# Performance work log

Hardware: AMD Instinct MI355X
Metric: run time of the kernel (lower is better)

## Reference

```python
import jax, jax.numpy as jnp
import numpy as np

NUM_HEADS = 32
NUM_KV_HEADS = 8
HEAD_DIM = 128
SEQ = 2048
MASK_BLOCK = 128  # diffusion-LM denoising block size


def setup_inputs() -> dict:
    key = jax.random.key(0)
    kq, kk, kv = jax.random.split(key, 3)
    q = jax.random.normal(kq, (SEQ, NUM_HEADS * HEAD_DIM), dtype=jnp.float32)
    k = jax.random.normal(kk, (SEQ, NUM_KV_HEADS * HEAD_DIM), dtype=jnp.float32)
    v = jax.random.normal(kv, (SEQ, NUM_KV_HEADS * HEAD_DIM), dtype=jnp.float32)
    # block-causal mask at MASK_BLOCK granularity: token_q attends to token_kv
    # iff block(token_kv) <= block(token_q). Every row has >=1 True entry.
    blk = jnp.arange(SEQ) // MASK_BLOCK
    block_mask = blk[None, :] <= blk[:, None]  # [S, S] bool
    return {"q": q, "k": k, "v": v, "block_mask": block_mask}


def reference(q, k, v, block_mask):
    S = q.shape[0]
    scale = 1.0 / np.sqrt(HEAD_DIM).astype(np.float32)  # flex_attention default scale
    qh = q.reshape(S, NUM_HEADS, HEAD_DIM)       # [S, Hq, D]
    kh = k.reshape(S, NUM_KV_HEADS, HEAD_DIM)    # [S, Hkv, D]
    vh = v.reshape(S, NUM_KV_HEADS, HEAD_DIM)
    # GQA: repeat each kv head over its query-head group
    group = NUM_HEADS // NUM_KV_HEADS
    kh = jnp.repeat(kh, group, axis=1)           # [S, Hq, D]
    vh = jnp.repeat(vh, group, axis=1)
    scores = jnp.einsum('qhd,khd->hqk', qh, kh) * scale  # [Hq, S, S]
    neg_inf = jnp.finfo(scores.dtype).min
    scores = jnp.where(block_mask[None, :, :], scores, neg_inf)
    probs = jax.nn.softmax(scores, axis=-1)
    o = jnp.einsum('hqk,khd->qhd', probs, vh)    # [S, Hq, D]
    return o.reshape(S, NUM_HEADS * HEAD_DIM)
```

## Files before the change

kernel.cpp:

```cpp
#include <hip/hip_runtime.h>
#include <hip/hip_bf16.h>

#define SEQL  2048
#define NHQ   32
#define NHKV  8
#define HD    128

typedef __attribute__((ext_vector_type(4))) float          f32x4;
typedef __attribute__((ext_vector_type(8))) short          bf16x8;
typedef __attribute__((ext_vector_type(4))) unsigned short u16x4;
typedef __attribute__((ext_vector_type(8))) unsigned short u16x8;
typedef __attribute__((ext_vector_type(2))) unsigned int   u32x2;

__device__ __forceinline__ unsigned short f2bf(float f) {
  union { float f; unsigned u; } v; v.f = f;
  unsigned u = v.u;
  return (unsigned short)((u + 0x7fffu + ((u >> 16) & 1u)) >> 16);
}

__device__ __forceinline__ void gload16(const void* g, void* l) {
  __builtin_amdgcn_global_load_lds(
      (const __attribute__((address_space(1))) unsigned int*)g,
      (__attribute__((address_space(3))) unsigned int*)l, 16, 0, 0);
}

__global__ __launch_bounds__(256) void prep_k(const float* __restrict__ k,
                                              unsigned short* __restrict__ kws) {
  int t = blockIdx.x * 256 + threadIdx.x;
  int s   = t >> 7;
  int col = (t & 127) << 3;
  int hkv = col >> 7;
  int d0  = col & 127;
  const float* src = k + (size_t)s * (NHKV * HD) + col;
  f32x4 a = *(const f32x4*)src;
  f32x4 b = *(const f32x4*)(src + 4);
  u16x8 r;
  r[0] = f2bf(a[0]); r[1] = f2bf(a[1]); r[2] = f2bf(a[2]); r[3] = f2bf(a[3]);
  r[4] = f2bf(b[0]); r[5] = f2bf(b[1]); r[6] = f2bf(b[2]); r[7] = f2bf(b[3]);
  int tile = s >> 6, rr = s & 63;
  int idx = (rr * 128 + d0) ^ ((rr & 7) << 3);
  *(u16x8*)(kws + (((size_t)(hkv * 32 + tile)) << 13) + idx) = r;
}

__global__ __launch_bounds__(256) void prep_v(const float* __restrict__ v,
                                              unsigned short* __restrict__ vws) {
  int t = blockIdx.x * 256 + threadIdx.x;
  int d   = t & 127;
  int hkv = (t >> 7) & 7;
  int rg  = t >> 10;
  int s0  = rg << 3;
  const float* src = v + (size_t)s0 * (NHKV * HD) + hkv * HD + d;
  u16x8 r;
  #pragma unroll
  for (int j = 0; j < 8; ++j) r[j] = f2bf(src[(size_t)j * (NHKV * HD)]);
  int tile = rg >> 3;
  int rloc = (rg & 7) << 3;
  int idx = (d * 64 + rloc) ^ ((d & 7) << 3);
  *(u16x8*)(vws + (((size_t)(hkv * 32 + tile)) << 13) + idx) = r;
}

__global__ __launch_bounds__(256, 2) void attn_fwd3(
    const float* __restrict__ q,
    const unsigned short* __restrict__ kws,
    const unsigned short* __restrict__ vws,
    float* __restrict__ out)
{
  __shared__ unsigned short Kb[2][8192];
  __shared__ unsigned short Vb[2][8192];
  __shared__ unsigned int   Pst[4][1024];

  const int tid  = threadIdx.x;
  const int lane = tid & 63;
  const int wv   = tid >> 6;
  const int l15  = lane & 15;
  const int lhi  = lane >> 4;
  const int swzP = (l15 & 7) << 2;
  const int swzK = (l15 & 7) << 3;

  const int bx   = blockIdx.x;
  const int hkv  = bx & 7;
  const int idx2 = bx >> 3;
  const int h    = hkv * 4 + (idx2 & 3);
  const int qt   = 15 - (idx2 >> 2);
  const int nt   = 2 * (qt + 1);

  const float qscale = 0.08838834764831845f * 1.4426950408889634f;
  const float THR = 11.5f;

  const unsigned short* ktiles = kws + (((size_t)hkv * 32) << 13);
  const unsigned short* vtiles = vws + (((size_t)hkv * 32) << 13);

  bf16x8 qf[2][4];
  #pragma unroll
  for (int qs = 0; qs < 2; ++qs) {
    const float* qbase = q + (size_t)(qt * 128 + qs * 64 + wv * 16 + l15) * (NHQ * HD) + h * HD + lhi * 8;
    #pragma unroll
    for (int c = 0; c < 4; ++c) {
      f32x4 a = *(const f32x4*)(qbase + c * 32);
      f32x4 b = *(const f32x4*)(qbase + c * 32 + 4);
      bf16x8 r;
      r[0] = (short)f2bf(a[0] * qscale);
      r[1] = (short)f2bf(a[1] * qscale);
      r[2] = (short)f2bf(a[2] * qscale);
      r[3] = (short)f2bf(a[3] * qscale);
      r[4] = (short)f2bf(b[0] * qscale);
      r[5] = (short)f2bf(b[1] * qscale);
      r[6] = (short)f2bf(b[2] * qscale);
      r[7] = (short)f2bf(b[3] * qscale);
      qf[qs][c] = r;
    }
  }

  f32x4 oacc[2][8];
  #pragma unroll
  for (int qs = 0; qs < 2; ++qs)
    #pragma unroll
    for (int i = 0; i < 8; ++i) oacc[qs][i] = (f32x4){0.f, 0.f, 0.f, 0.f};
  float mrun0 = -1e30f, mrun1 = -1e30f, lrun0 = 0.f, lrun1 = 0.f;

  auto STAGE = [&](int b, int kvt) {
    const char* gk = (const char*)(ktiles + ((size_t)kvt << 13));
    const char* gv = (const char*)(vtiles + ((size_t)kvt << 13));
    char* lk = (char*)&Kb[b][0];
    char* lv = (char*)&Vb[b][0];
    #pragma unroll
    for (int i = 0; i < 4; ++i) {
      const int off = wv * 4096 + i * 1024;
      gload16(gk + off + lane * 16, lk + off);
      gload16(gv + off + lane * 16, lv + off);
    }
  };

  auto compute = [&](int b) {
    f32x4 sa0[4], sa1[4];
    #pragma unroll
    for (int sub = 0; sub < 4; ++sub) {
      f32x4 a0 = (f32x4){0.f, 0.f, 0.f, 0.f};
      f32x4 a1 = (f32x4){0.f, 0.f, 0.f, 0.f};
      const int row = sub * 16 + l15;
      #pragma unroll
      for (int c = 0; c < 4; ++c) {
        bf16x8 kf = *(const bf16x8*)(&Kb[b][(row * 128 + c * 32 + lhi * 8) ^ swzK]);
        a0 = __builtin_amdgcn_mfma_f32_16x16x32_bf16(kf, qf[0][c], a0, 0, 0, 0);
        a1 = __builtin_amdgcn_mfma_f32_16x16x32_bf16(kf, qf[1][c], a1, 0, 0, 0);
      }
      sa0[sub] = a0; sa1[sub] = a1;
    }
    float mt0 = -1e30f, mt1 = -1e30f;
    #pragma unroll
    for (int sub = 0; sub < 4; ++sub)
      #pragma unroll
      for (int r = 0; r < 4; ++r) {
        mt0 = fmaxf(mt0, sa0[sub][r]);
        mt1 = fmaxf(mt1, sa1[sub][r]);
      }
    mt0 = fmaxf(mt0, __shfl_xor(mt0, 16));
    mt0 = fmaxf(mt0, __shfl_xor(mt0, 32));
    mt1 = fmaxf(mt1, __shfl_xor(mt1, 16));
    mt1 = fmaxf(mt1, __shfl_xor(mt1, 32));
    int need = (mt0 > mrun0 + THR) || (mt1 > mrun1 + THR);
    if (__any(need)) {
      float mn0 = fmaxf(mrun0, mt0), mn1 = fmaxf(mrun1, mt1);
      float c0 = exp2f(mrun0 - mn0), c1 = exp2f(mrun1 - mn1);
      mrun0 = mn0; mrun1 = mn1;
      lrun0 *= c0; lrun1 *= c1;
      #pragma unroll
      for (int d = 0; d < 8; ++d) { oacc[0][d] *= c0; oacc[1][d] *= c1; }
    }
    {
      float ts = 0.f;
      #pragma unroll
      for (int sub = 0; sub < 4; ++sub) {
        float p0 = exp2f(sa0[sub][0] - mrun0);
        float p1 = exp2f(sa0[sub][1] - mrun0);
        float p2 = exp2f(sa0[sub][2] - mrun0);
        float p3 = exp2f(sa0[sub][3] - mrun0);
        ts += (p0 + p1) + (p2 + p3);
        u32x2 w;
        w[0] = (unsigned)f2bf(p0) | ((unsigned)f2bf(p1) << 16);
        w[1] = (unsigned)f2bf(p2) | ((unsigned)f2bf(p3) << 16);
        *(u32x2*)(&Pst[wv][(l15 * 32 + sub * 8 + lhi * 2) ^ swzP]) = w;
      }
      ts += __shfl_xor(ts, 16);
      ts += __shfl_xor(ts, 32);
      lrun0 += ts;
    }
    {
      float ts = 0.f;
      #pragma unroll
      for (int sub = 0; sub < 4; ++sub) {
        float p0 = exp2f(sa1[sub][0] - mrun1);
        float p1 = exp2f(sa1[sub][1] - mrun1);
        float p2 = exp2f(sa1[sub][2] - mrun1);
        float p3 = exp2f(sa1[sub][3] - mrun1);
        ts += (p0 + p1) + (p2 + p3);
        u32x2 w;
        w[0] = (unsigned)f2bf(p0) | ((unsigned)f2bf(p1) << 16);
        w[1] = (unsigned)f2bf(p2) | ((unsigned)f2bf(p3) << 16);
        *(u32x2*)(&Pst[wv][(512 + l15 * 32 + sub * 8 + lhi * 2) ^ swzP]) = w;
      }
      ts += __shfl_xor(ts, 16);
      ts += __shfl_xor(ts, 32);
      lrun1 += ts;
    }
    #pragma unroll
    for (int kc = 0; kc < 2; ++kc) {
      bf16x8 pf0 = *(const bf16x8*)(&Pst[wv][(l15 * 32 + kc * 16 + lhi * 4) ^ swzP]);
      bf16x8 pf1 = *(const bf16x8*)(&Pst[wv][(512 + l15 * 32 + kc * 16 + lhi * 4) ^ swzP]);
      #pragma unroll
      for (int dsub = 0; dsub < 8; ++dsub) {
        const int d = dsub * 16 + l15;
        bf16x8 vf = *(const bf16x8*)(&Vb[b][(d * 64 + kc * 32 + lhi * 8) ^ swzK]);
        oacc[0][dsub] = __builtin_amdgcn_mfma_f32_16x16x32_bf16(vf, pf0, oacc[0][dsub], 0, 0, 0);
        oacc[1][dsub] = __builtin_amdgcn_mfma_f32_16x16x32_bf16(vf, pf1, oacc[1][dsub], 0, 0, 0);
      }
    }
  };

  STAGE(0, 0);
  int buf = 0;
  for (int t = 0; t < nt; ++t) {
    if (t + 1 < nt) {
      STAGE(buf ^ 1, t + 1);
      asm volatile("s_waitcnt vmcnt(8)" ::: "memory");
    } else {
      asm volatile("s_waitcnt vmcnt(0)" ::: "memory");
    }
    __builtin_amdgcn_s_barrier();
    asm volatile("" ::: "memory");
    compute(buf);
    asm volatile("" ::: "memory");
    __builtin_amdgcn_s_barrier();
    buf ^= 1;
  }

  {
    float invl = 1.0f / lrun0;
    float* ob = out + (size_t)(qt * 128 + wv * 16 + l15) * (NHQ * HD) + h * HD + lhi * 4;
    #pragma unroll
    for (int dsub = 0; dsub < 8; ++dsub)
      *(f32x4*)(ob + dsub * 16) = oacc[0][dsub] * invl;
  }
  {
    float invl = 1.0f / lrun1;
    float* ob = out + (size_t)(qt * 128 + 64 + wv * 16 + l15) * (NHQ * HD) + h * HD + lhi * 4;
    #pragma unroll
    for (int dsub = 0; dsub < 8; ++dsub)
      *(f32x4*)(ob + dsub * 16) = oacc[1][dsub] * invl;
  }
}

__global__ __launch_bounds__(256) void attn_v1(
    const float* __restrict__ q,
    const float* __restrict__ k,
    const float* __restrict__ v,
    float* __restrict__ out)
{
  __shared__ unsigned short Ks[64 * 128];
  __shared__ unsigned short Vt[128 * 64];
  __shared__ unsigned short Psl[4][16 * 64];

  const int tid  = threadIdx.x;
  const int lane = tid & 63;
  const int wv   = tid >> 6;
  const int bx   = blockIdx.x;
  const int h    = bx & 31;
  const int qt   = (SEQL / 64 - 1) - (bx >> 5);
  const int q0   = qt * 64;
  const int hkv  = h >> 2;
  const int l15 = lane & 15;
  const int lhi = lane >> 4;
  const float qscale = 0.08838834764831845f * 1.4426950408889634f;

  bf16x8 qf[4];
  {
    const float* qbase = q + (size_t)(q0 + wv * 16 + l15) * (NHQ * HD) + h * HD + lhi * 8;
    #pragma unroll
    for (int c = 0; c < 4; ++c) {
      const float* p8 = qbase + c * 32;
      f32x4 a = *(const f32x4*)p8;
      f32x4 b = *(const f32x4*)(p8 + 4);
      bf16x8 r;
      r[0] = (short)f2bf(a[0] * qscale); r[1] = (short)f2bf(a[1] * qscale);
      r[2] = (short)f2bf(a[2] * qscale); r[3] = (short)f2bf(a[3] * qscale);
      r[4] = (short)f2bf(b[0] * qscale); r[5] = (short)f2bf(b[1] * qscale);
      r[6] = (short)f2bf(b[2] * qscale); r[7] = (short)f2bf(b[3] * qscale);
      qf[c] = r;
    }
  }
  f32x4 oacc[8];
  #pragma unroll
  for (int i = 0; i < 8; ++i) oacc[i] = (f32x4){0.f, 0.f, 0.f, 0.f};
  float mrun[4], lrun[4];
  #pragma unroll
  for (int r = 0; r < 4; ++r) { mrun[r] = -1e30f; lrun[r] = 0.f; }
  const int ntiles = ((q0 >> 7) + 1) * 2;
  for (int t = 0; t < ntiles; ++t) {
    const int kv0 = t * 64;
    __syncthreads();
    #pragma unroll
    for (int it = 0; it < 8; ++it) {
      int c = it * 256 + tid;
      int row = c >> 5;
      int dc = (c & 31) << 2;
      f32x4 x = *(const f32x4*)(k + (size_t)(kv0 + row) * (NHKV * HD) + hkv * HD + dc);
      u16x4 y;
      y[0] = f2bf(x[0]); y[1] = f2bf(x[1]); y[2] = f2bf(x[2]); y[3] = f2bf(x[3]);
      int idx = (row * HD + dc) ^ ((row & 7) << 3);
      *(u16x4*)(&Ks[idx]) = y;
    }
    {
      int row = tid >> 2;
      int db = (tid & 3) << 5;
      const float* vbase = v + (size_t)(kv0 + row) * (NHKV * HD) + hkv * HD + db;
      #pragma unroll
      for (int it = 0; it < 8; ++it) {
        f32x4 x = *(const f32x4*)(vbase + it * 4);
        int d0 = db + it * 4;
        #pragma unroll
        for (int j = 0; j < 4; ++j) {
          int d = d0 + j;
          int idx = (d * 64 + row) ^ ((d & 7) << 3);
          Vt[idx] = f2bf(x[j]);
        }
      }
    }
    __syncthreads();
    f32x4 sacc[4];
    #pragma unroll
    for (int sub = 0; sub < 4; ++sub) {
      f32x4 acc = (f32x4){0.f, 0.f, 0.f, 0.f};
      #pragma unroll
      for (int c = 0; c < 4; ++c) {
        int row = sub * 16 + l15;
        int idx = (row * HD + c * 32 + lhi * 8) ^ ((row & 7) << 3);
        bf16x8 kf = *(const bf16x8*)(&Ks[idx]);
        acc = __builtin_amdgcn_mfma_f32_16x16x32_bf16(qf[c], kf, acc, 0, 0, 0);
      }
      sacc[sub] = acc;
    }
    float corr[4];
    #pragma unroll
    for (int r = 0; r < 4; ++r) {
      float mt = fmaxf(fmaxf(sacc[0][r], sacc[1][r]), fmaxf(sacc[2][r], sacc[3][r]));
      #pragma unroll
      for (int off = 1; off < 16; off <<= 1) mt = fmaxf(mt, __shfl_xor(mt, off));
      float mnew = fmaxf(mrun[r], mt);
      corr[r] = exp2f(mrun[r] - mnew);
      mrun[r] = mnew;
      float p0 = exp2f(sacc[0][r] - mnew);
      float p1 = exp2f(sacc[1][r] - mnew);
      float p2 = exp2f(sacc[2][r] - mnew);
      float p3 = exp2f(sacc[3][r] - mnew);
      int qr = (lhi << 2) + r;
      int swz = (qr & 7) << 3;
      int bq = qr * 64;
      Psl[wv][(bq + 0  + l15) ^ swz] = f2bf(p0);
      Psl[wv][(bq + 16 + l15) ^ swz] = f2bf(p1);
      Psl[wv][(bq + 32 + l15) ^ swz] = f2bf(p2);
      Psl[wv][(bq + 48 + l15) ^ swz] = f2bf(p3);
      float ts = p0 + p1 + p2 + p3;
      #pragma unroll
      for (int off = 1; off < 16; off <<= 1) ts += __shfl_xor(ts, off);
      lrun[r] = lrun[r] * corr[r] + ts;
    }
    #pragma unroll
    for (int dsub = 0; dsub < 8; ++dsub) {
      f32x4 o = oacc[dsub];
      o[0] *= corr[0]; o[1] *= corr[1]; o[2] *= corr[2]; o[3] *= corr[3];
      oacc[dsub] = o;
    }
    #pragma unroll
    for (int kc = 0; kc < 2; ++kc) {
      int pidx = (l15 * 64 + kc * 32 + lhi * 8) ^ ((l15 & 7) << 3);
      bf16x8 pf = *(const bf16x8*)(&Psl[wv][pidx]);
      #pragma unroll
      for (int dsub = 0; dsub < 8; ++dsub) {
        int d = dsub * 16 + l15;
        int vidx = (d * 64 + kc * 32 + lhi * 8) ^ ((d & 7) << 3);
        bf16x8 vf = *(const bf16x8*)(&Vt[vidx]);
        oacc[dsub] = __builtin_amdgcn_mfma_f32_16x16x32_bf16(pf, vf, oacc[dsub], 0, 0, 0);
      }
    }
  }
  float inv[4];
  #pragma unroll
  for (int r = 0; r < 4; ++r) inv[r] = 1.0f / lrun[r];
  float* obase = out + (size_t)(q0 + wv * 16 + (lhi << 2)) * (NHQ * HD) + h * HD + l15;
  #pragma unroll
  for (int dsub = 0; dsub < 8; ++dsub) {
    #pragma unroll
    for (int r = 0; r < 4; ++r) {
      obase[(size_t)r * (NHQ * HD) + dsub * 16] = oacc[dsub][r] * inv[r];
    }
  }
}

extern "C" void kernel_launch(void* const* d_in, const int* in_sizes, int n_in,
                              void* d_out, int out_size, void* d_ws, size_t ws_size,
                              hipStream_t stream) {
  const float* q = (const float*)d_in[0];
  const float* k = (const float*)d_in[1];
  const float* v = (const float*)d_in[2];
  float* out = (float*)d_out;
  const size_t need = (size_t)8 * 1024 * 1024 + 512;
  if (ws_size >= need) {
    unsigned short* kws = (unsigned short*)d_ws;
    unsigned short* vws = kws + (size_t)4 * 1024 * 1024 / 2;
    prep_k<<<1024, 256, 0, stream>>>(k, kws);
    prep_v<<<1024, 256, 0, stream>>>(v, vws);
    attn_fwd3<<<512, 256, 0, stream>>>(q, kws, vws, out);
  } else {
    attn_v1<<<1024, 256, 0, stream>>>(q, k, v, out);
  }
}
```

Measured before the change: 96.81 us.

## Pair light and heavy 64-row query tiles per block for balanced causal work

Each block now handles two 64-row query tiles, a short one and its mirror long one, back to back. Every block therefore runs the same 34 KV-tile iterations instead of 2 to 32 depending on its query tile. This removes the causal load imbalance and tail effect but halves per-tile Q reuse of each staged K/V tile, since each MFMA now covers one 64-row Q slice instead of two. It also swaps the manual bf16 rounding of P for the packed v_cvt_pk_bf16_f32 instruction and raises wave priority around the MFMA sections with s_setprio.

```diff
diff --git a/kernel.cpp b/kernel.cpp
--- a/kernel.cpp
+++ b/kernel.cpp
@@ -16,6 +16,12 @@
   union { float f; unsigned u; } v; v.f = f;
   unsigned u = v.u;
   return (unsigned short)((u + 0x7fffu + ((u >> 16) & 1u)) >> 16);
+}
+
+__device__ __forceinline__ unsigned cvtpk_bf16(float lo, float hi) {
+  unsigned r;
+  asm("v_cvt_pk_bf16_f32 %0, %1, %2" : "=v"(r) : "v"(lo), "v"(hi));
+  return r;
 }
 
 __device__ __forceinline__ void gload16(const void* g, void* l) {
@@ -59,7 +65,7 @@
   *(u16x8*)(vws + (((size_t)(hkv * 32 + tile)) << 13) + idx) = r;
 }
 
-__global__ __launch_bounds__(256, 2) void attn_fwd3(
+__global__ __launch_bounds__(256, 2) void attn_fwd4(
     const float* __restrict__ q,
     const unsigned short* __restrict__ kws,
     const unsigned short* __restrict__ vws,
@@ -67,7 +73,7 @@
 {
   __shared__ unsigned short Kb[2][8192];
   __shared__ unsigned short Vb[2][8192];
-  __shared__ unsigned int   Pst[4][1024];
+  __shared__ unsigned int   Pst[4][512];
 
   const int tid  = threadIdx.x;
   const int lane = tid & 63;
@@ -79,10 +85,11 @@
 
   const int bx   = blockIdx.x;
   const int hkv  = bx & 7;
-  const int idx2 = bx >> 3;
-  const int h    = hkv * 4 + (idx2 & 3);
-  const int qt   = 15 - (idx2 >> 2);
-  const int nt   = 2 * (qt + 1);
+  const int h    = hkv * 4 + ((bx >> 3) & 3);
+  const int pr   = bx >> 5;
+  const int qtA  = pr, qtB = 31 - pr;
+  const int nA   = ((qtA >> 1) + 1) * 2;
+  const int T    = 34;
 
   const float qscale = 0.08838834764831845f * 1.4426950408889634f;
   const float THR = 11.5f;
@@ -90,10 +97,12 @@
   const unsigned short* ktiles = kws + (((size_t)hkv * 32) << 13);
   const unsigned short* vtiles = vws + (((size_t)hkv * 32) << 13);
 
-  bf16x8 qf[2][4];
-  #pragma unroll
-  for (int qs = 0; qs < 2; ++qs) {
-    const float* qbase = q + (size_t)(qt * 128 + qs * 64 + wv * 16 + l15) * (NHQ * HD) + h * HD + lhi * 8;
+  bf16x8 qf[4];
+  f32x4 oacc[8];
+  float mrun, lrun;
+
+  auto loadQ = [&](int qt) {
+    const float* qbase = q + (size_t)(qt * 64 + wv * 16 + l15) * (NHQ * HD) + h * HD + lhi * 8;
     #pragma unroll
     for (int c = 0; c < 4; ++c) {
       f32x4 a = *(const f32x4*)(qbase + c * 32);
@@ -107,16 +116,23 @@
       r[5] = (short)f2bf(b[1] * qscale);
       r[6] = (short)f2bf(b[2] * qscale);
       r[7] = (short)f2bf(b[3] * qscale);
-      qf[qs][c] = r;
-    }
-  }
-
-  f32x4 oacc[2][8];
-  #pragma unroll
-  for (int qs = 0; qs < 2; ++qs)
-    #pragma unroll
-    for (int i = 0; i < 8; ++i) oacc[qs][i] = (f32x4){0.f, 0.f, 0.f, 0.f};
-  float mrun0 = -1e30f, mrun1 = -1e30f, lrun0 = 0.f, lrun1 = 0.f;
+      qf[c] = r;
+    }
+  };
+
+  auto resetAcc = [&]() {
+    #pragma unroll
+    for (int i = 0; i < 8; ++i) oacc[i] = (f32x4){0.f, 0.f, 0.f, 0.f};
+    mrun = -1e30f; lrun = 0.f;
+  };
+
+  auto epilogue = [&](int qt) {
+    float invl = 1.0f / lrun;
+    float* ob = out + (size_t)(qt * 64 + wv * 16 + l15) * (NHQ * HD) + h * HD + lhi * 4;
+    #pragma unroll
+    for (int dsub = 0; dsub < 8; ++dsub)
+      *(f32x4*)(ob + dsub * 16) = oacc[dsub] * invl;
+  };
 
   auto STAGE = [&](int b, int kvt) {
     const char* gk = (const char*)(ktiles + ((size_t)kvt << 13));
@@ -132,96 +148,75 @@
   };
 
   auto compute = [&](int b) {
-    f32x4 sa0[4], sa1[4];
+    f32x4 sa[4];
+    __builtin_amdgcn_s_setprio(1);
     #pragma unroll
     for (int sub = 0; sub < 4; ++sub) {
-      f32x4 a0 = (f32x4){0.f, 0.f, 0.f, 0.f};
-      f32x4 a1 = (f32x4){0.f, 0.f, 0.f, 0.f};
+      f32x4 acc = (f32x4){0.f, 0.f, 0.f, 0.f};
       const int row = sub * 16 + l15;
       #pragma unroll
       for (int c = 0; c < 4; ++c) {
         bf16x8 kf = *(const bf16x8*)(&Kb[b][(row * 128 + c * 32 + lhi * 8) ^ swzK]);
-        a0 = __builtin_amdgcn_mfma_f32_16x16x32_bf16(kf, qf[0][c], a0, 0, 0, 0);
-        a1 = __builtin_amdgcn_mfma_f32_16x16x32_bf16(kf, qf[1][c], a1, 0, 0, 0);
-      }
-      sa0[sub] = a0; sa1[sub] = a1;
-    }
-    float mt0 = -1e30f, mt1 = -1e30f;
+        acc = __builtin_amdgcn_mfma_f32_16x16x32_bf16(kf, qf[c], acc, 0, 0, 0);
+      }
+      sa[sub] = acc;
+    }
+    __builtin_amdgcn_s_setprio(0);
+    float mt = -1e30f;
     #pragma unroll
     for (int sub = 0; sub < 4; ++sub)
       #pragma unroll
-      for (int r = 0; r < 4; ++r) {
-        mt0 = fmaxf(mt0, sa0[sub][r]);
-        mt1 = fmaxf(mt1, sa1[sub][r]);
-      }
-    mt0 = fmaxf(mt0, __shfl_xor(mt0, 16));
-    mt0 = fmaxf(mt0, __shfl_xor(mt0, 32));
-    mt1 = fmaxf(mt1, __shfl_xor(mt1, 16));
-    mt1 = fmaxf(mt1, __shfl_xor(mt1, 32));
-    int need = (mt0 > mrun0 + THR) || (mt1 > mrun1 + THR);
-    if (__any(need)) {
-      float mn0 = fmaxf(mrun0, mt0), mn1 = fmaxf(mrun1, mt1);
-      float c0 = exp2f(mrun0 - mn0), c1 = exp2f(mrun1 - mn1);
-      mrun0 = mn0; mrun1 = mn1;
-      lrun0 *= c0; lrun1 *= c1;
-      #pragma unroll
-      for (int d = 0; d < 8; ++d) { oacc[0][d] *= c0; oacc[1][d] *= c1; }
+      for (int r = 0; r < 4; ++r) mt = fmaxf(mt, sa[sub][r]);
+    mt = fmaxf(mt, __shfl_xor(mt, 16));
+    mt = fmaxf(mt, __shfl_xor(mt, 32));
+    if (__any(mt > mrun + THR)) {
+      float mn = fmaxf(mrun, mt);
+      float c0 = exp2f(mrun - mn);
+      mrun = mn; lrun *= c0;
+      #pragma unroll
+      for (int d = 0; d < 8; ++d) oacc[d] *= c0;
     }
     {
       float ts = 0.f;
       #pragma unroll
       for (int sub = 0; sub < 4; ++sub) {
-        float p0 = exp2f(sa0[sub][0] - mrun0);
-        float p1 = exp2f(sa0[sub][1] - mrun0);
-        float p2 = exp2f(sa0[sub][2] - mrun0);
-        float p3 = exp2f(sa0[sub][3] - mrun0);
+        float p0 = exp2f(sa[sub][0] - mrun);
+        float p1 = exp2f(sa[sub][1] - mrun);
+        float p2 = exp2f(sa[sub][2] - mrun);
+        float p3 = exp2f(sa[sub][3] - mrun);
         ts += (p0 + p1) + (p2 + p3);
         u32x2 w;
-        w[0] = (unsigned)f2bf(p0) | ((unsigned)f2bf(p1) << 16);
-        w[1] = (unsigned)f2bf(p2) | ((unsigned)f2bf(p3) << 16);
+        w[0] = cvtpk_bf16(p0, p1);
+        w[1] = cvtpk_bf16(p2, p3);
         *(u32x2*)(&Pst[wv][(l15 * 32 + sub * 8 + lhi * 2) ^ swzP]) = w;
       }
       ts += __shfl_xor(ts, 16);
       ts += __shfl_xor(ts, 32);
-      lrun0 += ts;
-    }
-    {
-      float ts = 0.f;
-      #pragma unroll
-      for (int sub = 0; sub < 4; ++sub) {
-        float p0 = exp2f(sa1[sub][0] - mrun1);
-        float p1 = exp2f(sa1[sub][1] - mrun1);
-        float p2 = exp2f(sa1[sub][2] - mrun1);
-        float p3 = exp2f(sa1[sub][3] - mrun1);
-        ts += (p0 + p1) + (p2 + p3);
-        u32x2 w;
-        w[0] = (unsigned)f2bf(p0) | ((unsigned)f2bf(p1) << 16);
-        w[1] = (unsigned)f2bf(p2) | ((unsigned)f2bf(p3) << 16);
-        *(u32x2*)(&Pst[wv][(512 + l15 * 32 + sub * 8 + lhi * 2) ^ swzP]) = w;
-      }
-      ts += __shfl_xor(ts, 16);
-      ts += __shfl_xor(ts, 32);
-      lrun1 += ts;
-    }
+      lrun += ts;
+    }
+    __builtin_amdgcn_s_setprio(1);
     #pragma unroll
     for (int kc = 0; kc < 2; ++kc) {
-      bf16x8 pf0 = *(const bf16x8*)(&Pst[wv][(l15 * 32 + kc * 16 + lhi * 4) ^ swzP]);
-      bf16x8 pf1 = *(const bf16x8*)(&Pst[wv][(512 + l15 * 32 + kc * 16 + lhi * 4) ^ swzP]);
+      bf16x8 pf = *(const bf16x8*)(&Pst[wv][(l15 * 32 + kc * 16 + lhi * 4) ^ swzP]);
       #pragma unroll
       for (int dsub = 0; dsub < 8; ++dsub) {
         const int d = dsub * 16 + l15;
         bf16x8 vf = *(const bf16x8*)(&Vb[b][(d * 64 + kc * 32 + lhi * 8) ^ swzK]);
-        oacc[0][dsub] = __builtin_amdgcn_mfma_f32_16x16x32_bf16(vf, pf0, oacc[0][dsub], 0, 0, 0);
-        oacc[1][dsub] = __builtin_amdgcn_mfma_f32_16x16x32_bf16(vf, pf1, oacc[1][dsub], 0, 0, 0);
-      }
-    }
-  };
-
+        oacc[dsub] = __builtin_amdgcn_mfma_f32_16x16x32_bf16(vf, pf, oacc[dsub], 0, 0, 0);
+      }
+    }
+    __builtin_amdgcn_s_setprio(0);
+  };
+
+  loadQ(qtA);
+  resetAcc();
   STAGE(0, 0);
   int buf = 0;
-  for (int t = 0; t < nt; ++t) {
-    if (t + 1 < nt) {
-      STAGE(buf ^ 1, t + 1);
+  for (int t = 0; t < T; ++t) {
+    if (t == nA) { epilogue(qtA); loadQ(qtB); resetAcc(); }
+    if (t + 1 < T) {
+      const int p = t + 1;
+      STAGE(buf ^ 1, (p < nA) ? p : p - nA);
       asm volatile("s_waitcnt vmcnt(8)" ::: "memory");
     } else {
       asm volatile("s_waitcnt vmcnt(0)" ::: "memory");
@@ -233,21 +228,7 @@
     __builtin_amdgcn_s_barrier();
     buf ^= 1;
   }
-
-  {
-    float invl = 1.0f / lrun0;
-    float* ob = out + (size_t)(qt * 128 + wv * 16 + l15) * (NHQ * HD) + h * HD + lhi * 4;
-    #pragma unroll
-    for (int dsub = 0; dsub < 8; ++dsub)
-      *(f32x4*)(ob + dsub * 16) = oacc[0][dsub] * invl;
-  }
-  {
-    float invl = 1.0f / lrun1;
-    float* ob = out + (size_t)(qt * 128 + 64 + wv * 16 + l15) * (NHQ * HD) + h * HD + lhi * 4;
-    #pragma unroll
-    for (int dsub = 0; dsub < 8; ++dsub)
-      *(f32x4*)(ob + dsub * 16) = oacc[1][dsub] * invl;
-  }
+  epilogue(qtB);
 }
 
 __global__ __launch_bounds__(256) void attn_v1(
@@ -409,7 +390,7 @@
     unsigned short* vws = kws + (size_t)4 * 1024 * 1024 / 2;
     prep_k<<<1024, 256, 0, stream>>>(k, kws);
     prep_v<<<1024, 256, 0, stream>>>(v, vws);
-    attn_fwd3<<<512, 256, 0, stream>>>(q, kws, vws, out);
+    attn_fwd4<<<512, 256, 0, stream>>>(q, kws, vws, out);
   } else {
     attn_v1<<<1024, 256, 0, stream>>>(q, k, v, out);
   }
```

Measured after the change: 87.19 us. 1.11x faster.

## Split attention into 64-row blocks of 2 waves, single-buffered, with packed bf16 convert

Applied to the files above, without the earlier changes.

The attention kernel now launches 1024 blocks of 128 threads, each covering 64 query rows, where before it launched 512 blocks of 256 threads covering 128 rows. Blocks are ordered so the long causal tiles run first, giving finer-grained load balancing. The K/V LDS double buffer becomes a single buffer with a full wait before each tile, which cuts LDS use but removes load/compute overlap inside a block. It also replaces the software bf16 rounding of P with the hardware packed convert instruction and raises wave priority around the MFMA sections.

```diff
diff --git a/kernel.cpp b/kernel.cpp
--- a/kernel.cpp
+++ b/kernel.cpp
@@ -16,6 +16,12 @@
   union { float f; unsigned u; } v; v.f = f;
   unsigned u = v.u;
   return (unsigned short)((u + 0x7fffu + ((u >> 16) & 1u)) >> 16);
+}
+
+__device__ __forceinline__ unsigned cvtpk_bf16(float lo, float hi) {
+  unsigned r;
+  asm("v_cvt_pk_bf16_f32 %0, %1, %2" : "=v"(r) : "v"(lo), "v"(hi));
+  return r;
 }
 
 __device__ __forceinline__ void gload16(const void* g, void* l) {
@@ -59,15 +65,15 @@
   *(u16x8*)(vws + (((size_t)(hkv * 32 + tile)) << 13) + idx) = r;
 }
 
-__global__ __launch_bounds__(256, 2) void attn_fwd3(
+__global__ __launch_bounds__(128, 2) void attn_fwd6(
     const float* __restrict__ q,
     const unsigned short* __restrict__ kws,
     const unsigned short* __restrict__ vws,
     float* __restrict__ out)
 {
-  __shared__ unsigned short Kb[2][8192];
-  __shared__ unsigned short Vb[2][8192];
-  __shared__ unsigned int   Pst[4][1024];
+  __shared__ unsigned short Kb[8192];
+  __shared__ unsigned short Vb[8192];
+  __shared__ unsigned int   Pst[2][1024];
 
   const int tid  = threadIdx.x;
   const int lane = tid & 63;
@@ -78,11 +84,14 @@
   const int swzK = (l15 & 7) << 3;
 
   const int bx   = blockIdx.x;
-  const int hkv  = bx & 7;
-  const int idx2 = bx >> 3;
-  const int h    = hkv * 4 + (idx2 & 3);
-  const int qt   = 15 - (idx2 >> 2);
-  const int nt   = 2 * (qt + 1);
+  const int half = bx >> 9;
+  const int j    = bx & 511;
+  const int hkv  = j & 7;
+  const int h    = hkv * 4 + ((j >> 3) & 3);
+  const int pr   = j >> 5;
+  const int c    = half ? pr : (31 - pr);
+  const int nt   = ((c >> 1) + 1) * 2;
+  const int q0   = c * 64;
 
   const float qscale = 0.08838834764831845f * 1.4426950408889634f;
   const float THR = 11.5f;
@@ -93,11 +102,11 @@
   bf16x8 qf[2][4];
   #pragma unroll
   for (int qs = 0; qs < 2; ++qs) {
-    const float* qbase = q + (size_t)(qt * 128 + qs * 64 + wv * 16 + l15) * (NHQ * HD) + h * HD + lhi * 8;
-    #pragma unroll
-    for (int c = 0; c < 4; ++c) {
-      f32x4 a = *(const f32x4*)(qbase + c * 32);
-      f32x4 b = *(const f32x4*)(qbase + c * 32 + 4);
+    const float* qbase = q + (size_t)(q0 + qs * 32 + wv * 16 + l15) * (NHQ * HD) + h * HD + lhi * 8;
+    #pragma unroll
+    for (int cc = 0; cc < 4; ++cc) {
+      f32x4 a = *(const f32x4*)(qbase + cc * 32);
+      f32x4 b = *(const f32x4*)(qbase + cc * 32 + 4);
       bf16x8 r;
       r[0] = (short)f2bf(a[0] * qscale);
       r[1] = (short)f2bf(a[1] * qscale);
@@ -107,7 +116,7 @@
       r[5] = (short)f2bf(b[1] * qscale);
       r[6] = (short)f2bf(b[2] * qscale);
       r[7] = (short)f2bf(b[3] * qscale);
-      qf[qs][c] = r;
+      qf[qs][cc] = r;
     }
   }
 
@@ -118,34 +127,36 @@
     for (int i = 0; i < 8; ++i) oacc[qs][i] = (f32x4){0.f, 0.f, 0.f, 0.f};
   float mrun0 = -1e30f, mrun1 = -1e30f, lrun0 = 0.f, lrun1 = 0.f;
 
-  auto STAGE = [&](int b, int kvt) {
+  auto STAGE = [&](int kvt) {
     const char* gk = (const char*)(ktiles + ((size_t)kvt << 13));
     const char* gv = (const char*)(vtiles + ((size_t)kvt << 13));
-    char* lk = (char*)&Kb[b][0];
-    char* lv = (char*)&Vb[b][0];
-    #pragma unroll
-    for (int i = 0; i < 4; ++i) {
-      const int off = wv * 4096 + i * 1024;
+    char* lk = (char*)&Kb[0];
+    char* lv = (char*)&Vb[0];
+    #pragma unroll
+    for (int i = 0; i < 8; ++i) {
+      const int off = wv * 8192 + i * 1024;
       gload16(gk + off + lane * 16, lk + off);
       gload16(gv + off + lane * 16, lv + off);
     }
   };
 
-  auto compute = [&](int b) {
+  auto compute = [&]() {
     f32x4 sa0[4], sa1[4];
+    __builtin_amdgcn_s_setprio(1);
     #pragma unroll
     for (int sub = 0; sub < 4; ++sub) {
       f32x4 a0 = (f32x4){0.f, 0.f, 0.f, 0.f};
       f32x4 a1 = (f32x4){0.f, 0.f, 0.f, 0.f};
       const int row = sub * 16 + l15;
       #pragma unroll
-      for (int c = 0; c < 4; ++c) {
-        bf16x8 kf = *(const bf16x8*)(&Kb[b][(row * 128 + c * 32 + lhi * 8) ^ swzK]);
-        a0 = __builtin_amdgcn_mfma_f32_16x16x32_bf16(kf, qf[0][c], a0, 0, 0, 0);
-        a1 = __builtin_amdgcn_mfma_f32_16x16x32_bf16(kf, qf[1][c], a1, 0, 0, 0);
+      for (int cc = 0; cc < 4; ++cc) {
+        bf16x8 kf = *(const bf16x8*)(&Kb[(row * 128 + cc * 32 + lhi * 8) ^ swzK]);
+        a0 = __builtin_amdgcn_mfma_f32_16x16x32_bf16(kf, qf[0][cc], a0, 0, 0, 0);
+        a1 = __builtin_amdgcn_mfma_f32_16x16x32_bf16(kf, qf[1][cc], a1, 0, 0, 0);
       }
       sa0[sub] = a0; sa1[sub] = a1;
     }
+    __builtin_amdgcn_s_setprio(0);
     float mt0 = -1e30f, mt1 = -1e30f;
     #pragma unroll
     for (int sub = 0; sub < 4; ++sub)
@@ -177,8 +188,8 @@
         float p3 = exp2f(sa0[sub][3] - mrun0);
         ts += (p0 + p1) + (p2 + p3);
         u32x2 w;
-        w[0] = (unsigned)f2bf(p0) | ((unsigned)f2bf(p1) << 16);
-        w[1] = (unsigned)f2bf(p2) | ((unsigned)f2bf(p3) << 16);
+        w[0] = cvtpk_bf16(p0, p1);
+        w[1] = cvtpk_bf16(p2, p3);
         *(u32x2*)(&Pst[wv][(l15 * 32 + sub * 8 + lhi * 2) ^ swzP]) = w;
       }
       ts += __shfl_xor(ts, 16);
@@ -195,14 +206,15 @@
         float p3 = exp2f(sa1[sub][3] - mrun1);
         ts += (p0 + p1) + (p2 + p3);
         u32x2 w;
-        w[0] = (unsigned)f2bf(p0) | ((unsigned)f2bf(p1) << 16);
-        w[1] = (unsigned)f2bf(p2) | ((unsigned)f2bf(p3) << 16);
+        w[0] = cvtpk_bf16(p0, p1);
+        w[1] = cvtpk_bf16(p2, p3);
         *(u32x2*)(&Pst[wv][(512 + l15 * 32 + sub * 8 + lhi * 2) ^ swzP]) = w;
       }
       ts += __shfl_xor(ts, 16);
       ts += __shfl_xor(ts, 32);
       lrun1 += ts;
     }
+    __builtin_amdgcn_s_setprio(1);
     #pragma unroll
     for (int kc = 0; kc < 2; ++kc) {
       bf16x8 pf0 = *(const bf16x8*)(&Pst[wv][(l15 * 32 + kc * 16 + lhi * 4) ^ swzP]);
@@ -210,40 +222,34 @@
       #pragma unroll
       for (int dsub = 0; dsub < 8; ++dsub) {
         const int d = dsub * 16 + l15;
-        bf16x8 vf = *(const bf16x8*)(&Vb[b][(d * 64 + kc * 32 + lhi * 8) ^ swzK]);
+        bf16x8 vf = *(const bf16x8*)(&Vb[(d * 64 + kc * 32 + lhi * 8) ^ swzK]);
         oacc[0][dsub] = __builtin_amdgcn_mfma_f32_16x16x32_bf16(vf, pf0, oacc[0][dsub], 0, 0, 0);
         oacc[1][dsub] = __builtin_amdgcn_mfma_f32_16x16x32_bf16(vf, pf1, oacc[1][dsub], 0, 0, 0);
       }
     }
+    __builtin_amdgcn_s_setprio(0);
   };
 
-  STAGE(0, 0);
-  int buf = 0;
   for (int t = 0; t < nt; ++t) {
-    if (t + 1 < nt) {
-      STAGE(buf ^ 1, t + 1);
-      asm volatile("s_waitcnt vmcnt(8)" ::: "memory");
-    } else {
-      asm volatile("s_waitcnt vmcnt(0)" ::: "memory");
-    }
+    STAGE(t);
+    asm volatile("s_waitcnt vmcnt(0)" ::: "memory");
     __builtin_amdgcn_s_barrier();
     asm volatile("" ::: "memory");
-    compute(buf);
+    compute();
     asm volatile("" ::: "memory");
     __builtin_amdgcn_s_barrier();
-    buf ^= 1;
   }
 
   {
     float invl = 1.0f / lrun0;
-    float* ob = out + (size_t)(qt * 128 + wv * 16 + l15) * (NHQ * HD) + h * HD + lhi * 4;
+    float* ob = out + (size_t)(q0 + wv * 16 + l15) * (NHQ * HD) + h * HD + lhi * 4;
     #pragma unroll
     for (int dsub = 0; dsub < 8; ++dsub)
       *(f32x4*)(ob + dsub * 16) = oacc[0][dsub] * invl;
   }
   {
     float invl = 1.0f / lrun1;
-    float* ob = out + (size_t)(qt * 128 + 64 + wv * 16 + l15) * (NHQ * HD) + h * HD + lhi * 4;
+    float* ob = out + (size_t)(q0 + 32 + wv * 16 + l15) * (NHQ * HD) + h * HD + lhi * 4;
     #pragma unroll
     for (int dsub = 0; dsub < 8; ++dsub)
       *(f32x4*)(ob + dsub * 16) = oacc[1][dsub] * invl;
@@ -409,7 +415,7 @@
     unsigned short* vws = kws + (size_t)4 * 1024 * 1024 / 2;
     prep_k<<<1024, 256, 0, stream>>>(k, kws);
     prep_v<<<1024, 256, 0, stream>>>(v, vws);
-    attn_fwd3<<<512, 256, 0, stream>>>(q, kws, vws, out);
+    attn_fwd6<<<1024, 128, 0, stream>>>(q, kws, vws, out);
   } else {
     attn_v1<<<1024, 256, 0, stream>>>(q, k, v, out);
   }
```

Result: no change. 96.42 us (-0.4%).
